# Kernel tuning notes

Hardware: AMD Instinct MI355X
Metric: run time of the kernel (lower is better)

Reference implementation:

```python
import jax, jax.numpy as jnp
import numpy as np

CLARITY_K, CLARITY_SIGMA = 31, 8.0
TEXTURE_K, TEXTURE_SIGMA = 7, 1.5


def _gauss1d(size, sigma):
    grid = np.arange(size, dtype=np.float32) - size // 2
    g = np.exp(-grid ** 2 / (2.0 * sigma * sigma))
    return (g / g.sum()).astype(np.float32)


def _blur(img, g1d):
    # Separable Gaussian blur: the original 2D kernel is the outer product of
    # the normalized 1D gaussian with itself, so two 1D passes are exact.
    size = g1d.shape[0]
    pad = size // 2
    kh = jnp.asarray(g1d, img.dtype).reshape(1, 1, size, 1)  # OIHW, vertical
    kw = jnp.asarray(g1d, img.dtype).reshape(1, 1, 1, size)  # OIHW, horizontal
    dn = jax.lax.conv_dimension_numbers(img.shape, kh.shape, ('NCHW', 'OIHW', 'NCHW'))
    y = jax.lax.conv_general_dilated(img, kh, (1, 1), [(pad, pad), (0, 0)], dimension_numbers=dn)
    y = jax.lax.conv_general_dilated(y, kw, (1, 1), [(0, 0), (pad, pad)], dimension_numbers=dn)
    return y


def setup_inputs() -> dict:
    key = jax.random.key(0)
    kx, kc, kt = jax.random.split(key, 3)
    x = jax.random.uniform(kx, (8, 3, 1024, 1024), dtype=jnp.float32)
    clarity = jax.random.normal(kc, (), dtype=jnp.float32)
    texture = jax.random.normal(kt, (), dtype=jnp.float32)
    return {"x": x, "clarity": clarity, "texture": texture}


def reference(x, clarity, texture):
    g_clar = _gauss1d(CLARITY_K, CLARITY_SIGMA)
    g_tex = _gauss1d(TEXTURE_K, TEXTURE_SIGMA)

    # Rec.709 luma, shape [B,1,H,W]
    luma = 0.2126 * x[:, 0:1] + 0.7152 * x[:, 1:2] + 0.0722 * x[:, 2:3]

    mid_freq = luma - _blur(luma, g_clar)    # 31x31 gaussian
    high_freq = luma - _blur(luma, g_tex)    # 7x7 gaussian

    clarity_amount = jnp.tanh(clarity) * 0.5
    texture_amount = jnp.tanh(texture) * 0.3

    luma_enhanced = luma + clarity_amount * mid_freq + texture_amount * high_freq
    ratio = (luma_enhanced + 1e-6) / (luma + 1e-6)
    return jnp.clip(x * ratio, 0.0, 1.0)
```

## Files before the change

### kernel.cpp

```cpp
#include <hip/hip_runtime.h>
#include <hip/hip_fp16.h>
#include <cmath>

#define HH   1024
#define WW   1024
#define HW   (HH * WW)

#define SW   128
#define TH   64
#define T31R 94
#define T7R  70
#define STW  160

constexpr double cexp(double v) {
    double term = 1.0, sum = 1.0;
    for (int i = 1; i < 64; ++i) { term *= v / (double)i; sum += term; }
    return sum;
}
struct GW { float g31[31]; float g7[7]; };
constexpr GW make_gw() {
    GW r{};
    double t31[31]; double s31 = 0.0;
    for (int i = 0; i < 31; ++i) { double d = (double)(i - 15); t31[i] = cexp(-d * d / 128.0); s31 += t31[i]; }
    for (int i = 0; i < 31; ++i) r.g31[i] = (float)(t31[i] / s31);
    double t7[7]; double s7 = 0.0;
    for (int i = 0; i < 7; ++i) { double d = (double)(i - 3); t7[i] = cexp(-d * d / 4.5); s7 += t7[i]; }
    for (int i = 0; i < 7; ++i) r.g7[i] = (float)(t7[i] / s7);
    return r;
}
__constant__ GW GWC = make_gw();

__global__ __launch_bounds__(256, 3)
void fused_tile(const float* __restrict__ x,
                const float* __restrict__ clar,
                const float* __restrict__ tex,
                float* __restrict__ out) {
    __shared__ __align__(16) __half t31s[T31R][SW];
    __shared__ __align__(16) __half t7s [T7R][SW];
    __shared__ __align__(16) float stage[8][STW];

    const int id    = blockIdx.x;
    const int xcd   = id & 7;
    const int k     = id >> 3;
    const int combo = xcd * 8 + (k & 7);
    const int band  = k >> 3;
    const int img   = combo >> 3;
    const int strip = combo & 7;

    const int y0 = band * TH;
    const int x0 = strip * SW;
    const int t  = threadIdx.x;
    const int w  = t >> 6;
    const int l  = t & 63;

    const float* xb = x   + (size_t)img * 3 * HW;
    float*       ob = out + (size_t)img * 3 * HW;

    for (int it = 0; it < 12; ++it) {
        const int gbase = it * 8;

        #pragma unroll
        for (int cb = 0; cb < 2; ++cb) {
            const int c = t + 256 * cb;
            if (c < 320) {
                const int r  = c / 40;
                const int cc = c - 40 * r;
                const int tr = gbase + r;
                const int y  = y0 - 15 + tr;
                const int col = x0 - 16 + 4 * cc;
                float4 L = make_float4(0.f, 0.f, 0.f, 0.f);
                if (tr < T31R && (unsigned)y < (unsigned)HH && (unsigned)col < (unsigned)WW) {
                    const float* xr = xb + (size_t)y * WW + col;
                    const float4 R  = *(const float4*)(xr);
                    const float4 G  = *(const float4*)(xr + HW);
                    const float4 Bc = *(const float4*)(xr + 2 * HW);
                    L.x = fmaf(0.2126f, R.x, fmaf(0.7152f, G.x, 0.0722f * Bc.x));
                    L.y = fmaf(0.2126f, R.y, fmaf(0.7152f, G.y, 0.0722f * Bc.y));
                    L.z = fmaf(0.2126f, R.z, fmaf(0.7152f, G.z, 0.0722f * Bc.z));
                    L.w = fmaf(0.2126f, R.w, fmaf(0.7152f, G.w, 0.0722f * Bc.w));
                }
                if (r < 8) *(float4*)&stage[r][4 * cc] = L;
            }
        }
        __syncthreads();

        {
            const int lr = 2 * w + (l >> 5);
            const int tr = gbase + lr;
            const int c4 = (l & 31) * 4;
            if (tr < T31R) {
                float win[36];
                #pragma unroll
                for (int q = 0; q < 9; ++q)
                    *(float4*)&win[4 * q] = *(const float4*)&stage[lr][c4 + 4 * q];
                float o[4] = {0.f, 0.f, 0.f, 0.f};
                float p[4] = {0.f, 0.f, 0.f, 0.f};
                #pragma unroll
                for (int s = 0; s < 31; ++s) {
                    const float g = GWC.g31[s];
                    o[0] = fmaf(g, win[1 + s], o[0]);
                    o[1] = fmaf(g, win[2 + s], o[1]);
                    o[2] = fmaf(g, win[3 + s], o[2]);
                    o[3] = fmaf(g, win[4 + s], o[3]);
                }
                #pragma unroll
                for (int s = 0; s < 7; ++s) {
                    const float g = GWC.g7[s];
                    p[0] = fmaf(g, win[13 + s], p[0]);
                    p[1] = fmaf(g, win[14 + s], p[1]);
                    p[2] = fmaf(g, win[15 + s], p[2]);
                    p[3] = fmaf(g, win[16 + s], p[3]);
                }
                *(__half2*)&t31s[tr][c4]     = __floats2half2_rn(o[0], o[1]);
                *(__half2*)&t31s[tr][c4 + 2] = __floats2half2_rn(o[2], o[3]);
                if (tr >= 12 && tr < 12 + T7R) {
                    *(__half2*)&t7s[tr - 12][c4]     = __floats2half2_rn(p[0], p[1]);
                    *(__half2*)&t7s[tr - 12][c4 + 2] = __floats2half2_rn(p[2], p[3]);
                }
            }
        }
        __syncthreads();
    }

    const float ca = tanhf(clar[0]) * 0.5f;
    const float ta = tanhf(tex[0]) * 0.3f;

    const int cp = t & 63;
    const int rg = t >> 6;
    const int r0 = rg * 16;

    float2 w31[31];
    #pragma unroll
    for (int q = 0; q < 30; ++q)
        w31[q] = __half22float2(*(const __half2*)&t31s[r0 + q][2 * cp]);
    float2 w7[7];
    #pragma unroll
    for (int q = 0; q < 6; ++q)
        w7[q] = __half22float2(*(const __half2*)&t7s[r0 + q][2 * cp]);

    #pragma unroll
    for (int j = 0; j < 16; ++j) {
        w31[(30 + j) % 31] = __half22float2(*(const __half2*)&t31s[r0 + 30 + j][2 * cp]);
        w7 [(6 + j) % 7]   = __half22float2(*(const __half2*)&t7s [r0 + 6 + j][2 * cp]);

        float ax = 0.f, ay = 0.f;
        #pragma unroll
        for (int q = 0; q < 31; ++q) {
            const float g = GWC.g31[q];
            const float2 v = w31[(j + q) % 31];
            ax = fmaf(g, v.x, ax);
            ay = fmaf(g, v.y, ay);
        }
        float cx = 0.f, cy = 0.f;
        #pragma unroll
        for (int q = 0; q < 7; ++q) {
            const float g = GWC.g7[q];
            const float2 v = w7[(j + q) % 7];
            cx = fmaf(g, v.x, cx);
            cy = fmaf(g, v.y, cy);
        }

        const int y = y0 + r0 + j;
        const float* px = xb + (size_t)y * WW + x0 + 2 * cp;
        const float2 R  = *(const float2*)(px);
        const float2 G  = *(const float2*)(px + HW);
        const float2 Bc = *(const float2*)(px + 2 * HW);

        const float Lx  = fmaf(0.2126f, R.x, fmaf(0.7152f, G.x, 0.0722f * Bc.x));
        const float Ly  = fmaf(0.2126f, R.y, fmaf(0.7152f, G.y, 0.0722f * Bc.y));
        const float lex = Lx + ca * (Lx - ax) + ta * (Lx - cx);
        const float ley = Ly + ca * (Ly - ay) + ta * (Ly - cy);
        const float rx  = (lex + 1e-6f) / (Lx + 1e-6f);
        const float ry  = (ley + 1e-6f) / (Ly + 1e-6f);

        float2 Ro, Go, Bo;
        Ro.x = fminf(fmaxf(R.x  * rx, 0.f), 1.f);
        Ro.y = fminf(fmaxf(R.y  * ry, 0.f), 1.f);
        Go.x = fminf(fmaxf(G.x  * rx, 0.f), 1.f);
        Go.y = fminf(fmaxf(G.y  * ry, 0.f), 1.f);
        Bo.x = fminf(fmaxf(Bc.x * rx, 0.f), 1.f);
        Bo.y = fminf(fmaxf(Bc.y * ry, 0.f), 1.f);

        float* qo = ob + (size_t)y * WW + x0 + 2 * cp;
        *(float2*)(qo)          = Ro;
        *(float2*)(qo + HW)     = Go;
        *(float2*)(qo + 2 * HW) = Bo;
    }
}

extern "C" void kernel_launch(void* const* d_in, const int* in_sizes, int n_in,
                              void* d_out, int out_size, void* d_ws, size_t ws_size,
                              hipStream_t stream) {
    const float* x    = (const float*)d_in[0];
    const float* clar = (const float*)d_in[1];
    const float* tex  = (const float*)d_in[2];
    float* out = (float*)d_out;

    dim3 grid(8 * 8 * 16);
    dim3 block(256);
    hipLaunchKernelGGL(fused_tile, grid, block, 0, stream, x, clar, tex, out);
}
```

Measured before the change: 226.3 us.

## Reshape tiles to narrow tall strips with fp16 staging and higher occupancy

Changes the tile from 128 wide by 64 tall to 64 wide by 128 tall, so the vertical 31-tap halo overhead shrinks relative to the tile height while the horizontal halo grows. The luma staging buffer is stored as fp16 with 16 rows per iteration, cutting LDS use so launch bounds can request 4 blocks per SM. The final vertical pass now handles one column per thread over two row groups, with scalar global loads and stores instead of float2. The tradeoffs are more redundant horizontal-halo reads, narrower memory accesses, and extra fp16 rounding of the staged luma.

```diff
diff --git a/kernel.cpp b/kernel.cpp
--- a/kernel.cpp
+++ b/kernel.cpp
@@ -6,11 +6,12 @@
 #define WW   1024
 #define HW   (HH * WW)
 
-#define SW   128
-#define TH   64
-#define T31R 94
-#define T7R  70
-#define STW  160
+#define SW    64
+#define TH    128
+#define T31R  158
+#define T7R   134
+#define SROWS 16
+#define SPIT  96
 
 constexpr double cexp(double v) {
     double term = 1.0, sum = 1.0;
@@ -30,44 +31,42 @@
 }
 __constant__ GW GWC = make_gw();
 
-__global__ __launch_bounds__(256, 3)
+__global__ __launch_bounds__(256, 4)
 void fused_tile(const float* __restrict__ x,
                 const float* __restrict__ clar,
                 const float* __restrict__ tex,
                 float* __restrict__ out) {
-    __shared__ __align__(16) __half t31s[T31R][SW];
-    __shared__ __align__(16) __half t7s [T7R][SW];
-    __shared__ __align__(16) float stage[8][STW];
+    __shared__ __align__(16) __half t31s [T31R][SW];
+    __shared__ __align__(16) __half t7s  [T7R][SW];
+    __shared__ __align__(16) __half stage[SROWS][SPIT];
 
     const int id    = blockIdx.x;
     const int xcd   = id & 7;
     const int k     = id >> 3;
-    const int combo = xcd * 8 + (k & 7);
-    const int band  = k >> 3;
-    const int img   = combo >> 3;
-    const int strip = combo & 7;
+    const int combo = xcd * 16 + (k & 15);
+    const int band  = k >> 4;
+    const int img   = combo >> 4;
+    const int strip = combo & 15;
 
     const int y0 = band * TH;
     const int x0 = strip * SW;
     const int t  = threadIdx.x;
-    const int w  = t >> 6;
-    const int l  = t & 63;
 
     const float* xb = x   + (size_t)img * 3 * HW;
     float*       ob = out + (size_t)img * 3 * HW;
 
-    for (int it = 0; it < 12; ++it) {
-        const int gbase = it * 8;
+    for (int it = 0; it < 10; ++it) {
+        const int gbase = it * SROWS;
 
         #pragma unroll
-        for (int cb = 0; cb < 2; ++cb) {
-            const int c = t + 256 * cb;
-            if (c < 320) {
-                const int r  = c / 40;
-                const int cc = c - 40 * r;
-                const int tr = gbase + r;
-                const int y  = y0 - 15 + tr;
-                const int col = x0 - 16 + 4 * cc;
+        for (int s = 0; s < 2; ++s) {
+            const int u = t + 256 * s;
+            if (u < 384) {
+                const int r   = u / 24;
+                const int c8  = u - 24 * r;
+                const int tr  = gbase + r;
+                const int y   = y0 - 15 + tr;
+                const int col = x0 - 16 + 4 * c8;
                 float4 L = make_float4(0.f, 0.f, 0.f, 0.f);
                 if (tr < T31R && (unsigned)y < (unsigned)HH && (unsigned)col < (unsigned)WW) {
                     const float* xr = xb + (size_t)y * WW + col;
@@ -79,20 +78,29 @@
                     L.z = fmaf(0.2126f, R.z, fmaf(0.7152f, G.z, 0.0722f * Bc.z));
                     L.w = fmaf(0.2126f, R.w, fmaf(0.7152f, G.w, 0.0722f * Bc.w));
                 }
-                if (r < 8) *(float4*)&stage[r][4 * cc] = L;
+                union { float2 f; __half2 h[2]; } W;
+                W.h[0] = __floats2half2_rn(L.x, L.y);
+                W.h[1] = __floats2half2_rn(L.z, L.w);
+                *(float2*)&stage[r][4 * c8] = W.f;
             }
         }
         __syncthreads();
 
         {
-            const int lr = 2 * w + (l >> 5);
+            const int lr = t >> 4;
+            const int c  = t & 15;
             const int tr = gbase + lr;
-            const int c4 = (l & 31) * 4;
             if (tr < T31R) {
                 float win[36];
                 #pragma unroll
-                for (int q = 0; q < 9; ++q)
-                    *(float4*)&win[4 * q] = *(const float4*)&stage[lr][c4 + 4 * q];
+                for (int q = 0; q < 9; ++q) {
+                    union { float2 f; __half2 h[2]; } U;
+                    U.f = *(const float2*)&stage[lr][4 * c + 4 * q];
+                    const float2 a = __half22float2(U.h[0]);
+                    const float2 b = __half22float2(U.h[1]);
+                    win[4 * q]     = a.x; win[4 * q + 1] = a.y;
+                    win[4 * q + 2] = b.x; win[4 * q + 3] = b.y;
+                }
                 float o[4] = {0.f, 0.f, 0.f, 0.f};
                 float p[4] = {0.f, 0.f, 0.f, 0.f};
                 #pragma unroll
@@ -111,11 +119,15 @@
                     p[2] = fmaf(g, win[15 + s], p[2]);
                     p[3] = fmaf(g, win[16 + s], p[3]);
                 }
-                *(__half2*)&t31s[tr][c4]     = __floats2half2_rn(o[0], o[1]);
-                *(__half2*)&t31s[tr][c4 + 2] = __floats2half2_rn(o[2], o[3]);
+                union { float2 f; __half2 h[2]; } W;
+                W.h[0] = __floats2half2_rn(o[0], o[1]);
+                W.h[1] = __floats2half2_rn(o[2], o[3]);
+                *(float2*)&t31s[tr][4 * c] = W.f;
                 if (tr >= 12 && tr < 12 + T7R) {
-                    *(__half2*)&t7s[tr - 12][c4]     = __floats2half2_rn(p[0], p[1]);
-                    *(__half2*)&t7s[tr - 12][c4 + 2] = __floats2half2_rn(p[2], p[3]);
+                    union { float2 f; __half2 h[2]; } V;
+                    V.h[0] = __floats2half2_rn(p[0], p[1]);
+                    V.h[1] = __floats2half2_rn(p[2], p[3]);
+                    *(float2*)&t7s[tr - 12][4 * c] = V.f;
                 }
             }
         }
@@ -125,66 +137,48 @@
     const float ca = tanhf(clar[0]) * 0.5f;
     const float ta = tanhf(tex[0]) * 0.3f;
 
-    const int cp = t & 63;
-    const int rg = t >> 6;
-    const int r0 = rg * 16;
+    const int c = t & 63;
+    #pragma unroll
+    for (int s = 0; s < 2; ++s) {
+        const int rg = (t >> 6) + 4 * s;
+        const int r0 = rg * 16;
 
-    float2 w31[31];
-    #pragma unroll
-    for (int q = 0; q < 30; ++q)
-        w31[q] = __half22float2(*(const __half2*)&t31s[r0 + q][2 * cp]);
-    float2 w7[7];
-    #pragma unroll
-    for (int q = 0; q < 6; ++q)
-        w7[q] = __half22float2(*(const __half2*)&t7s[r0 + q][2 * cp]);
+        float w31[31];
+        #pragma unroll
+        for (int q = 0; q < 30; ++q) w31[q] = __half2float(t31s[r0 + q][c]);
+        float w7[7];
+        #pragma unroll
+        for (int q = 0; q < 6; ++q) w7[q] = __half2float(t7s[r0 + q][c]);
 
-    #pragma unroll
-    for (int j = 0; j < 16; ++j) {
-        w31[(30 + j) % 31] = __half22float2(*(const __half2*)&t31s[r0 + 30 + j][2 * cp]);
-        w7 [(6 + j) % 7]   = __half22float2(*(const __half2*)&t7s [r0 + 6 + j][2 * cp]);
+        #pragma unroll
+        for (int j = 0; j < 16; ++j) {
+            w31[(30 + j) % 31] = __half2float(t31s[r0 + 30 + j][c]);
+            w7 [(6 + j) % 7]   = __half2float(t7s [r0 + 6 + j][c]);
 
-        float ax = 0.f, ay = 0.f;
-        #pragma unroll
-        for (int q = 0; q < 31; ++q) {
-            const float g = GWC.g31[q];
-            const float2 v = w31[(j + q) % 31];
-            ax = fmaf(g, v.x, ax);
-            ay = fmaf(g, v.y, ay);
+            float a31 = 0.f;
+            #pragma unroll
+            for (int q = 0; q < 31; ++q)
+                a31 = fmaf(GWC.g31[q], w31[(j + q) % 31], a31);
+            float a7 = 0.f;
+            #pragma unroll
+            for (int q = 0; q < 7; ++q)
+                a7 = fmaf(GWC.g7[q], w7[(j + q) % 7], a7);
+
+            const int y = y0 + r0 + j;
+            const float* px = xb + (size_t)y * WW + x0 + c;
+            const float R  = px[0];
+            const float G  = px[HW];
+            const float Bc = px[2 * HW];
+
+            const float L     = fmaf(0.2126f, R, fmaf(0.7152f, G, 0.0722f * Bc));
+            const float le    = L + ca * (L - a31) + ta * (L - a7);
+            const float ratio = (le + 1e-6f) / (L + 1e-6f);
+
+            float* qo = ob + (size_t)y * WW + x0 + c;
+            qo[0]      = fminf(fmaxf(R  * ratio, 0.f), 1.f);
+            qo[HW]     = fminf(fmaxf(G  * ratio, 0.f), 1.f);
+            qo[2 * HW] = fminf(fmaxf(Bc * ratio, 0.f), 1.f);
         }
-        float cx = 0.f, cy = 0.f;
-        #pragma unroll
-        for (int q = 0; q < 7; ++q) {
-            const float g = GWC.g7[q];
-            const float2 v = w7[(j + q) % 7];
-            cx = fmaf(g, v.x, cx);
-            cy = fmaf(g, v.y, cy);
-        }
-
-        const int y = y0 + r0 + j;
-        const float* px = xb + (size_t)y * WW + x0 + 2 * cp;
-        const float2 R  = *(const float2*)(px);
-        const float2 G  = *(const float2*)(px + HW);
-        const float2 Bc = *(const float2*)(px + 2 * HW);
-
-        const float Lx  = fmaf(0.2126f, R.x, fmaf(0.7152f, G.x, 0.0722f * Bc.x));
-        const float Ly  = fmaf(0.2126f, R.y, fmaf(0.7152f, G.y, 0.0722f * Bc.y));
-        const float lex = Lx + ca * (Lx - ax) + ta * (Lx - cx);
-        const float ley = Ly + ca * (Ly - ay) + ta * (Ly - cy);
-        const float rx  = (lex + 1e-6f) / (Lx + 1e-6f);
-        const float ry  = (ley + 1e-6f) / (Ly + 1e-6f);
-
-        float2 Ro, Go, Bo;
-        Ro.x = fminf(fmaxf(R.x  * rx, 0.f), 1.f);
-        Ro.y = fminf(fmaxf(R.y  * ry, 0.f), 1.f);
-        Go.x = fminf(fmaxf(G.x  * rx, 0.f), 1.f);
-        Go.y = fminf(fmaxf(G.y  * ry, 0.f), 1.f);
-        Bo.x = fminf(fmaxf(Bc.x * rx, 0.f), 1.f);
-        Bo.y = fminf(fmaxf(Bc.y * ry, 0.f), 1.f);
-
-        float* qo = ob + (size_t)y * WW + x0 + 2 * cp;
-        *(float2*)(qo)          = Ro;
-        *(float2*)(qo + HW)     = Go;
-        *(float2*)(qo + 2 * HW) = Bo;
     }
 }
 
@@ -196,7 +190,7 @@
     const float* tex  = (const float*)d_in[2];
     float* out = (float*)d_out;
 
-    dim3 grid(8 * 8 * 16);
+    dim3 grid(8 * 16 * 8);
     dim3 block(256);
     hipLaunchKernelGGL(fused_tile, grid, block, 0, stream, x, clar, tex, out);
 }
```

Measured after the change: 198.9 us. 12.1% less time.
